# Kernel tuning notes

Measured on AMD Instinct MI355X. Metric: run time of the kernel, lower is better.

## Reference

```python
import jax, jax.numpy as jnp
import numpy as np

EPS = 1e-5

def _ln(x, g, b):
    m = jnp.mean(x, axis=-1, keepdims=True)
    v = jnp.mean(jnp.square(x - m), axis=-1, keepdims=True)
    return (x - m) * jax.lax.rsqrt(v + EPS) * g + b

def setup_inputs() -> dict:
    key = jax.random.key(0)
    ks = jax.random.split(key, 20)
    B, F = 262144, 768
    sizes = [F, 512, 256, 128, 1]  # LN(d_in) -> Linear(d_in, d_out) per block
    inp = {"input": jax.random.normal(ks[0], (B, F), dtype=jnp.float32)}
    for i in range(4):
        din, dout = sizes[i], sizes[i + 1]
        inp[f"g{i}"] = jnp.ones((din,), dtype=jnp.float32)
        inp[f"b{i}"] = jnp.zeros((din,), dtype=jnp.float32)
        bound = 1.0 / np.sqrt(din)
        inp[f"W{i}"] = jax.random.uniform(ks[1 + 2 * i], (dout, din), dtype=jnp.float32, minval=-bound, maxval=bound)
        inp[f"c{i}"] = jax.random.uniform(ks[2 + 2 * i], (dout,), dtype=jnp.float32, minval=-bound, maxval=bound)
    return inp

def reference(input, g0, b0, W0, c0, g1, b1, W1, c1, g2, b2, W2, c2, g3, b3, W3, c3):
    x = input
    params = [(g0, b0, W0, c0), (g1, b1, W1, c1), (g2, b2, W2, c2), (g3, b3, W3, c3)]
    for i, (g, b, W, c) in enumerate(params):
        x = _ln(x, g, b)
        x = x @ W.T + c
        if i != 3:
            x = jax.nn.elu(x)
    return jnp.squeeze(x, axis=-1)  # [B]
```

## Files before the change

### kernel.cpp

```cpp
#include <hip/hip_runtime.h>
#include <hip/hip_fp16.h>
#include <math.h>

typedef _Float16 half_t;
typedef half_t half4_t __attribute__((ext_vector_type(4)));
typedef half_t half8_t __attribute__((ext_vector_type(8)));
typedef float f32x4 __attribute__((ext_vector_type(4)));

#define LN_EPS 1e-5f

__global__ void pack_weights(const float* __restrict__ W0, const float* __restrict__ g0,
                             const float* __restrict__ W1, const float* __restrict__ g1,
                             const float* __restrict__ W2, const float* __restrict__ g2,
                             half_t* __restrict__ ws) {
    int sid = blockIdx.x * 256 + threadIdx.x;
    const float* W; const float* g; int K, T, off;
    if (sid < 49152)      { W = W0; g = g0; K = 768; T = 24; off = 0; }
    else if (sid < 65536) { W = W1; g = g1; K = 512; T = 16; off = 49152; sid -= 49152; }
    else if (sid < 69632) { W = W2; g = g2; K = 256; T = 8;  off = 65536; sid -= 65536; }
    else return;
    const int l   = sid & 63;
    const int t   = (sid >> 6) % T;
    const int cbg = (sid >> 6) / T;
    const int n   = (l & 15) + 16 * cbg;
    const int k0  = 32 * t + 8 * (l >> 4);
    const float* src = W + (size_t)n * K + k0;
    const float* gs  = g + k0;
    half8_t v;
    #pragma unroll
    for (int jq = 0; jq < 8; jq++) v[jq] = (half_t)(src[jq] * gs[jq]);
    *(half8_t*)(ws + (size_t)(off + sid) * 8) = v;
}

__global__ void fold_bias(const float* __restrict__ W0, const float* __restrict__ g0,
                          const float* __restrict__ b0, const float* __restrict__ c0,
                          const float* __restrict__ W1, const float* __restrict__ g1,
                          const float* __restrict__ b1, const float* __restrict__ c1,
                          const float* __restrict__ W2, const float* __restrict__ g2,
                          const float* __restrict__ b2, const float* __restrict__ c2,
                          const float* __restrict__ W3, const float* __restrict__ g3,
                          const float* __restrict__ b3, const float* __restrict__ c3,
                          float* __restrict__ f) {
    const int gw   = (blockIdx.x * 256 + threadIdx.x) >> 6;
    const int lane = threadIdx.x & 63;
    if (gw == 896) {
        float s = 0.f, cb_ = 0.f;
        for (int k = lane; k < 128; k += 64) {
            const float wg = W3[k] * g3[k];
            f[1792 + k] = wg;
            s += wg; cb_ += W3[k] * b3[k];
        }
        #pragma unroll
        for (int m = 1; m < 64; m <<= 1) { s += __shfl_xor(s, m); cb_ += __shfl_xor(cb_, m); }
        if (lane == 0) { f[1920] = s; f[1921] = cb_ + c3[0]; }
        return;
    }
    const float *W, *g, *b, *cc; int K, n; float *sf, *cf;
    if (gw < 512)      { W = W0; g = g0; b = b0; cc = c0; K = 768; n = gw;       sf = f;        cf = f + 512; }
    else if (gw < 768) { W = W1; g = g1; b = b1; cc = c1; K = 512; n = gw - 512; sf = f + 1024; cf = f + 1280; }
    else if (gw < 896) { W = W2; g = g2; b = b2; cc = c2; K = 256; n = gw - 768; sf = f + 1536; cf = f + 1664; }
    else return;
    const float* Wr = W + (size_t)n * K;
    float s = 0.f, cb_ = 0.f;
    for (int k = lane; k < K; k += 64) { const float wg = Wr[k] * g[k]; s += wg; cb_ += Wr[k] * b[k]; }
    #pragma unroll
    for (int m = 1; m < 64; m <<= 1) { s += __shfl_xor(s, m); cb_ += __shfl_xor(cb_, m); }
    if (lane == 0) { sf[n] = s; cf[n] = cb_ + cc[n]; }
}

__global__ __launch_bounds__(512, 4)
void fused_mlp(const float* __restrict__ x_in,
               const half_t* __restrict__ W0p, const half_t* __restrict__ W1p,
               const half_t* __restrict__ W2p, const float* __restrict__ f,
               float* __restrict__ out)
{
    __shared__ half_t frag[32768];
    __shared__ float psum[8][64], psq[8][64], pdot[8][64];
    __shared__ float row_m[64], row_rs[64];

    const int tid  = threadIdx.x;
    const int lane = tid & 63;
    const int wv   = tid >> 6;
    const int grp  = lane >> 4;
    const int cl   = lane & 15;
    const int row  = tid >> 3;
    const int jj   = tid & 7;
    const int rbw  = row >> 4;
    const long r0  = (long)blockIdx.x * 64;
    const float* xrow = x_in + (r0 + row) * 768;

    const float* s0f = f;        const float* c0f = f + 512;
    const float* s1f = f + 1024; const float* c1f = f + 1280;
    const float* s2f = f + 1536; const float* c2f = f + 1664;
    const float* w3f = f + 1792;

    float s = 0.f, ss = 0.f;
    f32x4 vb[4];

    auto stage_load = [&](int c) {
        const float* xp = xrow + 128 * c + 4 * jj;
        #pragma unroll
        for (int i = 0; i < 4; i++)
            vb[i] = __builtin_nontemporal_load((const f32x4*)(xp + 32 * i));
    };
    auto stage_write = [&](int c) {
        half_t* fb = frag + 8192 * (c & 1);
        const int hg = jj >> 1, jo = 4 * (jj & 1);
        #pragma unroll
        for (int i = 0; i < 4; i++) {
            const f32x4 v = vb[i];
            s  += v[0] + v[1] + v[2] + v[3];
            ss += v[0]*v[0] + v[1]*v[1] + v[2]*v[2] + v[3]*v[3];
            half4_t hv;
            hv[0] = (half_t)v[0]; hv[1] = (half_t)v[1];
            hv[2] = (half_t)v[2]; hv[3] = (half_t)v[3];
            *(half4_t*)(&fb[((i * 4 + rbw) * 64 + ((row & 15) + 16 * hg)) * 8 + jo]) = hv;
        }
    };

    f32x4 acc0[4][4];
    #pragma unroll
    for (int rb = 0; rb < 4; rb++)
        #pragma unroll
        for (int cb = 0; cb < 4; cb++) acc0[rb][cb] = 0.f;

    auto gemm0 = [&](int c) {
        const half_t* fb = frag + 8192 * (c & 1);
        const half_t* wp = W0p + (size_t)(4 * wv * 24 + 4 * c) * 512 + lane * 8;
        half8_t bA[4], bB[4];
        #pragma unroll
        for (int cb = 0; cb < 4; cb++) bA[cb] = *(const half8_t*)(wp + cb * 12288);
        #pragma unroll
        for (int tt = 0; tt < 4; tt++) {
            half8_t* cur = (tt & 1) ? bB : bA;
            half8_t* nxt = (tt & 1) ? bA : bB;
            if (tt < 3) {
                #pragma unroll
                for (int cb = 0; cb < 4; cb++)
                    nxt[cb] = *(const half8_t*)(wp + (tt + 1) * 512 + cb * 12288);
            }
            half8_t af[4];
            #pragma unroll
            for (int rb = 0; rb < 4; rb++)
                af[rb] = *(const half8_t*)(&fb[((tt * 4 + rb) * 64 + lane) * 8]);
            #pragma unroll
            for (int cb = 0; cb < 4; cb++)
                #pragma unroll
                for (int rb = 0; rb < 4; rb++)
                    acc0[rb][cb] = __builtin_amdgcn_mfma_f32_16x16x32_f16(af[rb], cur[cb], acc0[rb][cb], 0, 0, 0);
        }
    };

    stage_load(0); stage_write(0);
    __syncthreads();
    #pragma unroll 1
    for (int c = 0; c < 6; c++) {
        if (c < 5) stage_load(c + 1);
        gemm0(c);
        if (c < 5) stage_write(c + 1);
        if (c == 4) {
            s  += __shfl_xor(s, 1);  s  += __shfl_xor(s, 2);  s  += __shfl_xor(s, 4);
            ss += __shfl_xor(ss, 1); ss += __shfl_xor(ss, 2); ss += __shfl_xor(ss, 4);
            if (jj == 0) {
                const float mm = s * (1.f / 768.f);
                row_m[row]  = mm;
                row_rs[row] = 1.f / sqrtf(ss * (1.f / 768.f) - mm * mm + LN_EPS);
            }
        }
        __syncthreads();
    }

    {
        float sv[4], cv[4];
        #pragma unroll
        for (int cb = 0; cb < 4; cb++) {
            const int c = cl + 16 * (4 * wv + cb);
            sv[cb] = s0f[c]; cv[cb] = c0f[c];
        }
        #pragma unroll
        for (int rb = 0; rb < 4; rb++)
            #pragma unroll
            for (int v = 0; v < 4; v++) {
                const int r = 16 * rb + 4 * grp + v;
                const float rm = row_m[r], rr = row_rs[r];
                float a_ = 0.f, q_ = 0.f;
                #pragma unroll
                for (int cb = 0; cb < 4; cb++) {
                    float y = rr * (acc0[rb][cb][v] - rm * sv[cb]) + cv[cb];
                    y = y > 0.f ? y : (__expf(y) - 1.f);
                    acc0[rb][cb][v] = y;
                    a_ += y; q_ += y * y;
                }
                a_ += __shfl_xor(a_, 1); a_ += __shfl_xor(a_, 2); a_ += __shfl_xor(a_, 4); a_ += __shfl_xor(a_, 8);
                q_ += __shfl_xor(q_, 1); q_ += __shfl_xor(q_, 2); q_ += __shfl_xor(q_, 4); q_ += __shfl_xor(q_, 8);
                if (cl == 0) { psum[wv][r] = a_; psq[wv][r] = q_; }
            }
        #pragma unroll
        for (int cb = 0; cb < 4; cb++) {
            const int c = cl + 16 * (4 * wv + cb);
            const int t = c >> 5, j = c & 7, sc = 16 * ((c >> 3) & 3);
            #pragma unroll
            for (int rb = 0; rb < 4; rb++)
                #pragma unroll
                for (int v = 0; v < 4; v++)
                    frag[((t * 4 + rb) * 64 + (4 * grp + v + sc)) * 8 + j] = (half_t)acc0[rb][cb][v];
        }
    }
    __syncthreads();
    if (tid < 64) {
        float a_ = 0.f, q_ = 0.f;
        #pragma unroll
        for (int w = 0; w < 8; w++) { a_ += psum[w][tid]; q_ += psq[w][tid]; }
        const float mm = a_ * (1.f / 512.f);
        row_m[tid]  = mm;
        row_rs[tid] = 1.f / sqrtf(q_ * (1.f / 512.f) - mm * mm + LN_EPS);
    }
    __syncthreads();

    f32x4 acc1[4][2];
    #pragma unroll
    for (int rb = 0; rb < 4; rb++) { acc1[rb][0] = 0.f; acc1[rb][1] = 0.f; }
    {
        const half_t* wp = W1p + (size_t)(2 * wv * 16) * 512 + lane * 8;
        half8_t bA[2], bB[2];
        bA[0] = *(const half8_t*)(wp);
        bA[1] = *(const half8_t*)(wp + 8192);
        #pragma unroll
        for (int t = 0; t < 16; t++) {
            half8_t* cur = (t & 1) ? bB : bA;
            half8_t* nxt = (t & 1) ? bA : bB;
            if (t < 15) {
                nxt[0] = *(const half8_t*)(wp + (t + 1) * 512);
                nxt[1] = *(const half8_t*)(wp + (t + 1) * 512 + 8192);
            }
            half8_t af[4];
            #pragma unroll
            for (int rb = 0; rb < 4; rb++)
                af[rb] = *(const half8_t*)(&frag[((t * 4 + rb) * 64 + lane) * 8]);
            #pragma unroll
            for (int cb = 0; cb < 2; cb++)
                #pragma unroll
                for (int rb = 0; rb < 4; rb++)
                    acc1[rb][cb] = __builtin_amdgcn_mfma_f32_16x16x32_f16(af[rb], cur[cb], acc1[rb][cb], 0, 0, 0);
        }
    }

    {
        float sv[2], cv[2];
        #pragma unroll
        for (int cb = 0; cb < 2; cb++) {
            const int c = cl + 16 * (2 * wv + cb);
            sv[cb] = s1f[c]; cv[cb] = c1f[c];
        }
        #pragma unroll
        for (int rb = 0; rb < 4; rb++)
            #pragma unroll
            for (int v = 0; v < 4; v++) {
                const int r = 16 * rb + 4 * grp + v;
                const float rm = row_m[r], rr = row_rs[r];
                float a_ = 0.f, q_ = 0.f;
                #pragma unroll
                for (int cb = 0; cb < 2; cb++) {
                    float y = rr * (acc1[rb][cb][v] - rm * sv[cb]) + cv[cb];
                    y = y > 0.f ? y : (__expf(y) - 1.f);
                    acc1[rb][cb][v] = y;
                    a_ += y; q_ += y * y;
                }
                a_ += __shfl_xor(a_, 1); a_ += __shfl_xor(a_, 2); a_ += __shfl_xor(a_, 4); a_ += __shfl_xor(a_, 8);
                q_ += __shfl_xor(q_, 1); q_ += __shfl_xor(q_, 2); q_ += __shfl_xor(q_, 4); q_ += __shfl_xor(q_, 8);
                if (cl == 0) { psum[wv][r] = a_; psq[wv][r] = q_; }
            }
    }
    __syncthreads();
    #pragma unroll
    for (int cb = 0; cb < 2; cb++) {
        const int c = cl + 16 * (2 * wv + cb);
        const int t = c >> 5, j = c & 7, sc = 16 * ((c >> 3) & 3);
        #pragma unroll
        for (int rb = 0; rb < 4; rb++)
            #pragma unroll
            for (int v = 0; v < 4; v++)
                frag[((t * 4 + rb) * 64 + (4 * grp + v + sc)) * 8 + j] = (half_t)acc1[rb][cb][v];
    }
    if (tid < 64) {
        float a_ = 0.f, q_ = 0.f;
        #pragma unroll
        for (int w = 0; w < 8; w++) { a_ += psum[w][tid]; q_ += psq[w][tid]; }
        const float mm = a_ * (1.f / 256.f);
        row_m[tid]  = mm;
        row_rs[tid] = 1.f / sqrtf(q_ * (1.f / 256.f) - mm * mm + LN_EPS);
    }
    __syncthreads();

    f32x4 acc2[4];
    #pragma unroll
    for (int rb = 0; rb < 4; rb++) acc2[rb] = 0.f;
    {
        const half_t* wp = W2p + (size_t)(wv * 8) * 512 + lane * 8;
        half8_t bA = *(const half8_t*)(wp);
        #pragma unroll
        for (int t = 0; t < 8; t++) {
            const half8_t cur = bA;
            if (t < 7) bA = *(const half8_t*)(wp + (t + 1) * 512);
            half8_t af[4];
            #pragma unroll
            for (int rb = 0; rb < 4; rb++)
                af[rb] = *(const half8_t*)(&frag[((t * 4 + rb) * 64 + lane) * 8]);
            #pragma unroll
            for (int rb = 0; rb < 4; rb++)
                acc2[rb] = __builtin_amdgcn_mfma_f32_16x16x32_f16(af[rb], cur, acc2[rb], 0, 0, 0);
        }
    }

    {
        const int c2i = cl + 16 * wv;
        const float sv = s2f[c2i], cv = c2f[c2i], w3v = w3f[c2i];
        #pragma unroll
        for (int rb = 0; rb < 4; rb++)
            #pragma unroll
            for (int v = 0; v < 4; v++) {
                const int r = 16 * rb + 4 * grp + v;
                const float rm = row_m[r], rr = row_rs[r];
                float y = rr * (acc2[rb][v] - rm * sv) + cv;
                y = y > 0.f ? y : (__expf(y) - 1.f);
                float a_ = y, q_ = y * y, d_ = y * w3v;
                a_ += __shfl_xor(a_, 1); a_ += __shfl_xor(a_, 2); a_ += __shfl_xor(a_, 4); a_ += __shfl_xor(a_, 8);
                q_ += __shfl_xor(q_, 1); q_ += __shfl_xor(q_, 2); q_ += __shfl_xor(q_, 4); q_ += __shfl_xor(q_, 8);
                d_ += __shfl_xor(d_, 1); d_ += __shfl_xor(d_, 2); d_ += __shfl_xor(d_, 4); d_ += __shfl_xor(d_, 8);
                if (cl == 0) { psum[wv][r] = a_; psq[wv][r] = q_; pdot[wv][r] = d_; }
            }
    }
    __syncthreads();
    if (tid < 64) {
        float a_ = 0.f, q_ = 0.f, d_ = 0.f;
        #pragma unroll
        for (int w = 0; w < 8; w++) { a_ += psum[w][tid]; q_ += psq[w][tid]; d_ += pdot[w][tid]; }
        const float mm = a_ * (1.f / 128.f);
        const float rs = 1.f / sqrtf(q_ * (1.f / 128.f) - mm * mm + LN_EPS);
        out[r0 + tid] = rs * (d_ - mm * f[1920]) + f[1921];
    }
}

extern "C" void kernel_launch(void* const* d_in, const int* in_sizes, int n_in,
                              void* d_out, int out_size, void* d_ws, size_t ws_size,
                              hipStream_t stream) {
    const float* x  = (const float*)d_in[0];
    const float* g0 = (const float*)d_in[1];
    const float* b0 = (const float*)d_in[2];
    const float* W0 = (const float*)d_in[3];
    const float* c0 = (const float*)d_in[4];
    const float* g1 = (const float*)d_in[5];
    const float* b1 = (const float*)d_in[6];
    const float* W1 = (const float*)d_in[7];
    const float* c1 = (const float*)d_in[8];
    const float* g2 = (const float*)d_in[9];
    const float* b2 = (const float*)d_in[10];
    const float* W2 = (const float*)d_in[11];
    const float* c2 = (const float*)d_in[12];
    const float* g3 = (const float*)d_in[13];
    const float* b3 = (const float*)d_in[14];
    const float* W3 = (const float*)d_in[15];
    const float* c3 = (const float*)d_in[16];

    half_t* ws = (half_t*)d_ws;
    float*  f  = (float*)(ws + 557056);

    pack_weights<<<272, 256, 0, stream>>>(W0, g0, W1, g1, W2, g2, ws);
    fold_bias<<<225, 256, 0, stream>>>(W0, g0, b0, c0, W1, g1, b1, c1,
                                       W2, g2, b2, c2, W3, g3, b3, c3, f);

    const int nrows = in_sizes[0] / 768;
    fused_mlp<<<nrows / 64, 512, 0, stream>>>(
        x, ws, ws + 393216, ws + 524288, f, (float*)d_out);
}
```

Measured before the change: 577.7 us.

## Compute per-row LayerNorm stats from half-precision LDS fragments instead of shuffles

Per-row mean and variance for the next LayerNorm are now computed after activations are written to shared memory. Eight threads per row read the half-precision fragments and reduce with 3-step shuffles, replacing per-wave 4-step shuffle reductions plus cross-wave partial-sum arrays and a serial 64-thread combine. This removes a block barrier per layer and the single-wave tail reduction, but it adds LDS reads and uses fp16-rounded values for the statistics. The final layer stages outputs in a padded LDS tile and caches the last weight vector in shared memory.

```diff
diff --git a/kernel.cpp b/kernel.cpp
--- a/kernel.cpp
+++ b/kernel.cpp
@@ -75,8 +75,8 @@
                float* __restrict__ out)
 {
     __shared__ half_t frag[32768];
-    __shared__ float psum[8][64], psq[8][64], pdot[8][64];
     __shared__ float row_m[64], row_rs[64];
+    __shared__ float w3s[128];
 
     const int tid  = threadIdx.x;
     const int lane = tid & 63;
@@ -92,7 +92,8 @@
     const float* s0f = f;        const float* c0f = f + 512;
     const float* s1f = f + 1024; const float* c1f = f + 1280;
     const float* s2f = f + 1536; const float* c2f = f + 1664;
-    const float* w3f = f + 1792;
+
+    if (tid < 128) w3s[tid] = f[1792 + tid];
 
     float s = 0.f, ss = 0.f;
     f32x4 vb[4];
@@ -183,17 +184,11 @@
             for (int v = 0; v < 4; v++) {
                 const int r = 16 * rb + 4 * grp + v;
                 const float rm = row_m[r], rr = row_rs[r];
-                float a_ = 0.f, q_ = 0.f;
                 #pragma unroll
                 for (int cb = 0; cb < 4; cb++) {
                     float y = rr * (acc0[rb][cb][v] - rm * sv[cb]) + cv[cb];
-                    y = y > 0.f ? y : (__expf(y) - 1.f);
-                    acc0[rb][cb][v] = y;
-                    a_ += y; q_ += y * y;
+                    acc0[rb][cb][v] = y > 0.f ? y : (__expf(y) - 1.f);
                 }
-                a_ += __shfl_xor(a_, 1); a_ += __shfl_xor(a_, 2); a_ += __shfl_xor(a_, 4); a_ += __shfl_xor(a_, 8);
-                q_ += __shfl_xor(q_, 1); q_ += __shfl_xor(q_, 2); q_ += __shfl_xor(q_, 4); q_ += __shfl_xor(q_, 8);
-                if (cl == 0) { psum[wv][r] = a_; psq[wv][r] = q_; }
             }
         #pragma unroll
         for (int cb = 0; cb < 4; cb++) {
@@ -207,15 +202,26 @@
         }
     }
     __syncthreads();
-    if (tid < 64) {
-        float a_ = 0.f, q_ = 0.f;
-        #pragma unroll
-        for (int w = 0; w < 8; w++) { a_ += psum[w][tid]; q_ += psq[w][tid]; }
-        const float mm = a_ * (1.f / 512.f);
-        row_m[tid]  = mm;
-        row_rs[tid] = 1.f / sqrtf(q_ * (1.f / 512.f) - mm * mm + LN_EPS);
-    }
-    __syncthreads();
+
+    {
+        const int r15 = row & 15, rb = row >> 4;
+        float s_ = 0.f, q_ = 0.f;
+        #pragma unroll
+        for (int i = 0; i < 8; i++) {
+            const int ch = jj + 8 * i;
+            const int t = ch >> 2, cg = ch & 3;
+            const half8_t h = *(const half8_t*)(frag + (size_t)((t * 4 + rb) * 64 + r15 + 16 * cg) * 8);
+            #pragma unroll
+            for (int e = 0; e < 8; e++) { const float fv = (float)h[e]; s_ += fv; q_ += fv * fv; }
+        }
+        s_ += __shfl_xor(s_, 1); s_ += __shfl_xor(s_, 2); s_ += __shfl_xor(s_, 4);
+        q_ += __shfl_xor(q_, 1); q_ += __shfl_xor(q_, 2); q_ += __shfl_xor(q_, 4);
+        if (jj == 0) {
+            const float mm = s_ * (1.f / 512.f);
+            row_m[row]  = mm;
+            row_rs[row] = 1.f / sqrtf(q_ * (1.f / 512.f) - mm * mm + LN_EPS);
+        }
+    }
 
     f32x4 acc1[4][2];
     #pragma unroll
@@ -244,6 +250,7 @@
                     acc1[rb][cb] = __builtin_amdgcn_mfma_f32_16x16x32_f16(af[rb], cur[cb], acc1[rb][cb], 0, 0, 0);
         }
     }
+    __syncthreads();
 
     {
         float sv[2], cv[2];
@@ -258,39 +265,44 @@
             for (int v = 0; v < 4; v++) {
                 const int r = 16 * rb + 4 * grp + v;
                 const float rm = row_m[r], rr = row_rs[r];
-                float a_ = 0.f, q_ = 0.f;
                 #pragma unroll
                 for (int cb = 0; cb < 2; cb++) {
                     float y = rr * (acc1[rb][cb][v] - rm * sv[cb]) + cv[cb];
-                    y = y > 0.f ? y : (__expf(y) - 1.f);
-                    acc1[rb][cb][v] = y;
-                    a_ += y; q_ += y * y;
+                    acc1[rb][cb][v] = y > 0.f ? y : (__expf(y) - 1.f);
                 }
-                a_ += __shfl_xor(a_, 1); a_ += __shfl_xor(a_, 2); a_ += __shfl_xor(a_, 4); a_ += __shfl_xor(a_, 8);
-                q_ += __shfl_xor(q_, 1); q_ += __shfl_xor(q_, 2); q_ += __shfl_xor(q_, 4); q_ += __shfl_xor(q_, 8);
-                if (cl == 0) { psum[wv][r] = a_; psq[wv][r] = q_; }
-            }
-    }
-    __syncthreads();
-    #pragma unroll
-    for (int cb = 0; cb < 2; cb++) {
-        const int c = cl + 16 * (2 * wv + cb);
-        const int t = c >> 5, j = c & 7, sc = 16 * ((c >> 3) & 3);
-        #pragma unroll
-        for (int rb = 0; rb < 4; rb++)
-            #pragma unroll
-            for (int v = 0; v < 4; v++)
-                frag[((t * 4 + rb) * 64 + (4 * grp + v + sc)) * 8 + j] = (half_t)acc1[rb][cb][v];
-    }
-    if (tid < 64) {
-        float a_ = 0.f, q_ = 0.f;
-        #pragma unroll
-        for (int w = 0; w < 8; w++) { a_ += psum[w][tid]; q_ += psq[w][tid]; }
-        const float mm = a_ * (1.f / 256.f);
-        row_m[tid]  = mm;
-        row_rs[tid] = 1.f / sqrtf(q_ * (1.f / 256.f) - mm * mm + LN_EPS);
-    }
-    __syncthreads();
+            }
+        #pragma unroll
+        for (int cb = 0; cb < 2; cb++) {
+            const int c = cl + 16 * (2 * wv + cb);
+            const int t = c >> 5, j = c & 7, sc = 16 * ((c >> 3) & 3);
+            #pragma unroll
+            for (int rb = 0; rb < 4; rb++)
+                #pragma unroll
+                for (int v = 0; v < 4; v++)
+                    frag[((t * 4 + rb) * 64 + (4 * grp + v + sc)) * 8 + j] = (half_t)acc1[rb][cb][v];
+        }
+    }
+    __syncthreads();
+
+    {
+        const int r15 = row & 15, rb = row >> 4;
+        float s_ = 0.f, q_ = 0.f;
+        #pragma unroll
+        for (int i = 0; i < 4; i++) {
+            const int ch = jj + 8 * i;
+            const int t = ch >> 2, cg = ch & 3;
+            const half8_t h = *(const half8_t*)(frag + (size_t)((t * 4 + rb) * 64 + r15 + 16 * cg) * 8);
+            #pragma unroll
+            for (int e = 0; e < 8; e++) { const float fv = (float)h[e]; s_ += fv; q_ += fv * fv; }
+        }
+        s_ += __shfl_xor(s_, 1); s_ += __shfl_xor(s_, 2); s_ += __shfl_xor(s_, 4);
+        q_ += __shfl_xor(q_, 1); q_ += __shfl_xor(q_, 2); q_ += __shfl_xor(q_, 4);
+        if (jj == 0) {
+            const float mm = s_ * (1.f / 256.f);
+            row_m[row]  = mm;
+            row_rs[row] = 1.f / sqrtf(q_ * (1.f / 256.f) - mm * mm + LN_EPS);
+        }
+    }
 
     f32x4 acc2[4];
     #pragma unroll
@@ -311,10 +323,11 @@
                 acc2[rb] = __builtin_amdgcn_mfma_f32_16x16x32_f16(af[rb], cur, acc2[rb], 0, 0, 0);
         }
     }
+    __syncthreads();
 
     {
         const int c2i = cl + 16 * wv;
-        const float sv = s2f[c2i], cv = c2f[c2i], w3v = w3f[c2i];
+        const float sv = s2f[c2i], cv = c2f[c2i];
         #pragma unroll
         for (int rb = 0; rb < 4; rb++)
             #pragma unroll
@@ -323,21 +336,31 @@
                 const float rm = row_m[r], rr = row_rs[r];
                 float y = rr * (acc2[rb][v] - rm * sv) + cv;
                 y = y > 0.f ? y : (__expf(y) - 1.f);
-                float a_ = y, q_ = y * y, d_ = y * w3v;
-                a_ += __shfl_xor(a_, 1); a_ += __shfl_xor(a_, 2); a_ += __shfl_xor(a_, 4); a_ += __shfl_xor(a_, 8);
-                q_ += __shfl_xor(q_, 1); q_ += __shfl_xor(q_, 2); q_ += __shfl_xor(q_, 4); q_ += __shfl_xor(q_, 8);
-                d_ += __shfl_xor(d_, 1); d_ += __shfl_xor(d_, 2); d_ += __shfl_xor(d_, 4); d_ += __shfl_xor(d_, 8);
-                if (cl == 0) { psum[wv][r] = a_; psq[wv][r] = q_; pdot[wv][r] = d_; }
-            }
-    }
-    __syncthreads();
-    if (tid < 64) {
-        float a_ = 0.f, q_ = 0.f, d_ = 0.f;
-        #pragma unroll
-        for (int w = 0; w < 8; w++) { a_ += psum[w][tid]; q_ += psq[w][tid]; d_ += pdot[w][tid]; }
-        const float mm = a_ * (1.f / 128.f);
-        const float rs = 1.f / sqrtf(q_ * (1.f / 128.f) - mm * mm + LN_EPS);
-        out[r0 + tid] = rs * (d_ - mm * f[1920]) + f[1921];
+                frag[r * 136 + c2i] = (half_t)y;
+            }
+    }
+    __syncthreads();
+
+    {
+        float s_ = 0.f, q_ = 0.f, d_ = 0.f;
+        #pragma unroll
+        for (int u = 0; u < 2; u++) {
+            const int cb = jj * 16 + 8 * u;
+            const half8_t h = *(const half8_t*)(frag + row * 136 + cb);
+            #pragma unroll
+            for (int e = 0; e < 8; e++) {
+                const float fv = (float)h[e];
+                s_ += fv; q_ += fv * fv; d_ += fv * w3s[cb + e];
+            }
+        }
+        s_ += __shfl_xor(s_, 1); s_ += __shfl_xor(s_, 2); s_ += __shfl_xor(s_, 4);
+        q_ += __shfl_xor(q_, 1); q_ += __shfl_xor(q_, 2); q_ += __shfl_xor(q_, 4);
+        d_ += __shfl_xor(d_, 1); d_ += __shfl_xor(d_, 2); d_ += __shfl_xor(d_, 4);
+        if (jj == 0) {
+            const float mm = s_ * (1.f / 128.f);
+            const float rs = 1.f / sqrtf(q_ * (1.f / 128.f) - mm * mm + LN_EPS);
+            out[r0 + row] = rs * (d_ - mm * f[1920]) + f[1921];
+        }
     }
 }
 
```

Result: faster. 548.0 us (-5.1%).

## Process two row tiles per block, overlapping tile B loads with tile A tail layers

Applied to the files above, without the earlier changes.

Each block now handles 128 rows as two 64-row tiles. The layer-1/2/3 GEMMs and epilogues of tile A are interleaved with the streaming x loads and layer-0 GEMM chunks of tile B, so the memory-bound input stream overlaps the small tail layers. The LN0 statistics and the final LN3/dot are computed with fp16 fdot2 instead of fp32 FMAs, and the last layer's reduction now goes through shared memory rather than shuffles plus a cross-wave reduction. Occupancy hint drops to 2 blocks per CU and LDS grows, and fp16 statistics accumulation may reduce accuracy.

```diff
diff --git a/kernel.cpp b/kernel.cpp
--- a/kernel.cpp
+++ b/kernel.cpp
@@ -3,11 +3,13 @@
 #include <math.h>
 
 typedef _Float16 half_t;
+typedef half_t half2_t __attribute__((ext_vector_type(2)));
 typedef half_t half4_t __attribute__((ext_vector_type(4)));
 typedef half_t half8_t __attribute__((ext_vector_type(8)));
 typedef float f32x4 __attribute__((ext_vector_type(4)));
 
 #define LN_EPS 1e-5f
+#define FDOT2(a, b, c) __builtin_amdgcn_fdot2((a), (b), (c), false)
 
 __global__ void pack_weights(const float* __restrict__ W0, const float* __restrict__ g0,
                              const float* __restrict__ W1, const float* __restrict__ g1,
@@ -68,15 +70,17 @@
     if (lane == 0) { sf[n] = s; cf[n] = cb_ + cc[n]; }
 }
 
-__global__ __launch_bounds__(512, 4)
+__global__ __launch_bounds__(512, 2)
 void fused_mlp(const float* __restrict__ x_in,
                const half_t* __restrict__ W0p, const half_t* __restrict__ W1p,
                const half_t* __restrict__ W2p, const float* __restrict__ f,
                float* __restrict__ out)
 {
-    __shared__ half_t frag[32768];
-    __shared__ float psum[8][64], psq[8][64], pdot[8][64];
-    __shared__ float row_m[64], row_rs[64];
+    __shared__ half_t xreg[32768];
+    __shared__ half_t stg2[16384];
+    __shared__ float rmA[64], rsA[64], rmB[64], rsB[64];
+    __shared__ float ps[8][64], pq[8][64];
+    __shared__ half2_t w3h[64];
 
     const int tid  = threadIdx.x;
     const int lane = tid & 63;
@@ -86,46 +90,64 @@
     const int row  = tid >> 3;
     const int jj   = tid & 7;
     const int rbw  = row >> 4;
-    const long r0  = (long)blockIdx.x * 64;
-    const float* xrow = x_in + (r0 + row) * 768;
+    const long r0  = (long)blockIdx.x * 128;
+    const float* xrA = x_in + (r0 + row) * 768;
+    const float* xrB = xrA + 64 * 768;
 
     const float* s0f = f;        const float* c0f = f + 512;
     const float* s1f = f + 1024; const float* c1f = f + 1280;
     const float* s2f = f + 1536; const float* c2f = f + 1664;
-    const float* w3f = f + 1792;
-
-    float s = 0.f, ss = 0.f;
+    const half2_t one2 = {(half_t)1.f, (half_t)1.f};
+
+    if (tid < 64) {
+        half2_t w; w[0] = (half_t)f[1792 + 2 * tid]; w[1] = (half_t)f[1793 + 2 * tid];
+        w3h[tid] = w;
+    }
+
+    float sA = 0.f, ssA = 0.f, sB = 0.f, ssB = 0.f;
     f32x4 vb[4];
-
-    auto stage_load = [&](int c) {
-        const float* xp = xrow + 128 * c + 4 * jj;
+    f32x4 acc0[4][4];
+    f32x4 acc1[4][2];
+    f32x4 acc2[4];
+
+    auto zacc0 = [&]() {
+        #pragma unroll
+        for (int rb = 0; rb < 4; rb++)
+            #pragma unroll
+            for (int cb = 0; cb < 4; cb++) acc0[rb][cb] = 0.f;
+    };
+
+    auto stage_load = [&](const float* xr, int c) {
+        const float* xp = xr + 128 * c + 4 * jj;
         #pragma unroll
         for (int i = 0; i < 4; i++)
             vb[i] = __builtin_nontemporal_load((const f32x4*)(xp + 32 * i));
     };
-    auto stage_write = [&](int c) {
-        half_t* fb = frag + 8192 * (c & 1);
+    auto stage_write = [&](int c, float& s_, float& ss_) {
+        half_t* fb = stg2 + 8192 * (c & 1);
         const int hg = jj >> 1, jo = 4 * (jj & 1);
         #pragma unroll
         for (int i = 0; i < 4; i++) {
             const f32x4 v = vb[i];
-            s  += v[0] + v[1] + v[2] + v[3];
-            ss += v[0]*v[0] + v[1]*v[1] + v[2]*v[2] + v[3]*v[3];
-            half4_t hv;
-            hv[0] = (half_t)v[0]; hv[1] = (half_t)v[1];
-            hv[2] = (half_t)v[2]; hv[3] = (half_t)v[3];
+            half2_t h01; h01[0] = (half_t)v[0]; h01[1] = (half_t)v[1];
+            half2_t h23; h23[0] = (half_t)v[2]; h23[1] = (half_t)v[3];
+            s_  = FDOT2(h01, one2, s_);  s_  = FDOT2(h23, one2, s_);
+            ss_ = FDOT2(h01, h01, ss_);  ss_ = FDOT2(h23, h23, ss_);
+            half4_t hv; hv[0] = h01[0]; hv[1] = h01[1]; hv[2] = h23[0]; hv[3] = h23[1];
             *(half4_t*)(&fb[((i * 4 + rbw) * 64 + ((row & 15) + 16 * hg)) * 8 + jo]) = hv;
         }
     };
-
-    f32x4 acc0[4][4];
-    #pragma unroll
-    for (int rb = 0; rb < 4; rb++)
-        #pragma unroll
-        for (int cb = 0; cb < 4; cb++) acc0[rb][cb] = 0.f;
-
-    auto gemm0 = [&](int c) {
-        const half_t* fb = frag + 8192 * (c & 1);
+    auto ln0_fin = [&](float& s_, float& ss_, float* rm, float* rs) {
+        s_  += __shfl_xor(s_, 1);  s_  += __shfl_xor(s_, 2);  s_  += __shfl_xor(s_, 4);
+        ss_ += __shfl_xor(ss_, 1); ss_ += __shfl_xor(ss_, 2); ss_ += __shfl_xor(ss_, 4);
+        if (jj == 0) {
+            const float mm = s_ * (1.f / 768.f);
+            rm[row] = mm;
+            rs[row] = 1.f / sqrtf(ss_ * (1.f / 768.f) - mm * mm + LN_EPS);
+        }
+    };
+    auto gemm0c = [&](int c) {
+        const half_t* fb = stg2 + 8192 * (c & 1);
         const half_t* wp = W0p + (size_t)(4 * wv * 24 + 4 * c) * 512 + lane * 8;
         half8_t bA[4], bB[4];
         #pragma unroll
@@ -150,27 +172,7 @@
                     acc0[rb][cb] = __builtin_amdgcn_mfma_f32_16x16x32_f16(af[rb], cur[cb], acc0[rb][cb], 0, 0, 0);
         }
     };
-
-    stage_load(0); stage_write(0);
-    __syncthreads();
-    #pragma unroll 1
-    for (int c = 0; c < 6; c++) {
-        if (c < 5) stage_load(c + 1);
-        gemm0(c);
-        if (c < 5) stage_write(c + 1);
-        if (c == 4) {
-            s  += __shfl_xor(s, 1);  s  += __shfl_xor(s, 2);  s  += __shfl_xor(s, 4);
-            ss += __shfl_xor(ss, 1); ss += __shfl_xor(ss, 2); ss += __shfl_xor(ss, 4);
-            if (jj == 0) {
-                const float mm = s * (1.f / 768.f);
-                row_m[row]  = mm;
-                row_rs[row] = 1.f / sqrtf(ss * (1.f / 768.f) - mm * mm + LN_EPS);
-            }
-        }
-        __syncthreads();
-    }
-
-    {
+    auto ep0 = [&](const float* rm0, const float* rs0) {
         float sv[4], cv[4];
         #pragma unroll
         for (int cb = 0; cb < 4; cb++) {
@@ -182,7 +184,7 @@
             #pragma unroll
             for (int v = 0; v < 4; v++) {
                 const int r = 16 * rb + 4 * grp + v;
-                const float rm = row_m[r], rr = row_rs[r];
+                const float rm = rm0[r], rr = rs0[r];
                 float a_ = 0.f, q_ = 0.f;
                 #pragma unroll
                 for (int cb = 0; cb < 4; cb++) {
@@ -193,7 +195,7 @@
                 }
                 a_ += __shfl_xor(a_, 1); a_ += __shfl_xor(a_, 2); a_ += __shfl_xor(a_, 4); a_ += __shfl_xor(a_, 8);
                 q_ += __shfl_xor(q_, 1); q_ += __shfl_xor(q_, 2); q_ += __shfl_xor(q_, 4); q_ += __shfl_xor(q_, 8);
-                if (cl == 0) { psum[wv][r] = a_; psq[wv][r] = q_; }
+                if (cl == 0) { ps[wv][r] = a_; pq[wv][r] = q_; }
             }
         #pragma unroll
         for (int cb = 0; cb < 4; cb++) {
@@ -203,24 +205,22 @@
             for (int rb = 0; rb < 4; rb++)
                 #pragma unroll
                 for (int v = 0; v < 4; v++)
-                    frag[((t * 4 + rb) * 64 + (4 * grp + v + sc)) * 8 + j] = (half_t)acc0[rb][cb][v];
-        }
-    }
-    __syncthreads();
-    if (tid < 64) {
-        float a_ = 0.f, q_ = 0.f;
-        #pragma unroll
-        for (int w = 0; w < 8; w++) { a_ += psum[w][tid]; q_ += psq[w][tid]; }
-        const float mm = a_ * (1.f / 512.f);
-        row_m[tid]  = mm;
-        row_rs[tid] = 1.f / sqrtf(q_ * (1.f / 512.f) - mm * mm + LN_EPS);
-    }
-    __syncthreads();
-
-    f32x4 acc1[4][2];
-    #pragma unroll
-    for (int rb = 0; rb < 4; rb++) { acc1[rb][0] = 0.f; acc1[rb][1] = 0.f; }
-    {
+                    xreg[((t * 4 + rb) * 64 + (4 * grp + v + sc)) * 8 + j] = (half_t)acc0[rb][cb][v];
+        }
+    };
+    auto combine = [&](float* rm, float* rs, float inv) {
+        if (tid < 64) {
+            float a_ = 0.f, q_ = 0.f;
+            #pragma unroll
+            for (int w = 0; w < 8; w++) { a_ += ps[w][tid]; q_ += pq[w][tid]; }
+            const float mm = a_ * inv;
+            rm[tid] = mm;
+            rs[tid] = 1.f / sqrtf(q_ * inv - mm * mm + LN_EPS);
+        }
+    };
+    auto gemm1 = [&]() {
+        #pragma unroll
+        for (int rb = 0; rb < 4; rb++) { acc1[rb][0] = 0.f; acc1[rb][1] = 0.f; }
         const half_t* wp = W1p + (size_t)(2 * wv * 16) * 512 + lane * 8;
         half8_t bA[2], bB[2];
         bA[0] = *(const half8_t*)(wp);
@@ -236,16 +236,15 @@
             half8_t af[4];
             #pragma unroll
             for (int rb = 0; rb < 4; rb++)
-                af[rb] = *(const half8_t*)(&frag[((t * 4 + rb) * 64 + lane) * 8]);
+                af[rb] = *(const half8_t*)(&xreg[((t * 4 + rb) * 64 + lane) * 8]);
             #pragma unroll
             for (int cb = 0; cb < 2; cb++)
                 #pragma unroll
                 for (int rb = 0; rb < 4; rb++)
                     acc1[rb][cb] = __builtin_amdgcn_mfma_f32_16x16x32_f16(af[rb], cur[cb], acc1[rb][cb], 0, 0, 0);
         }
-    }
-
-    {
+    };
+    auto ep1 = [&](const float* rm1, const float* rs1) {
         float sv[2], cv[2];
         #pragma unroll
         for (int cb = 0; cb < 2; cb++) {
@@ -257,7 +256,7 @@
             #pragma unroll
             for (int v = 0; v < 4; v++) {
                 const int r = 16 * rb + 4 * grp + v;
-                const float rm = row_m[r], rr = row_rs[r];
+                const float rm = rm1[r], rr = rs1[r];
                 float a_ = 0.f, q_ = 0.f;
                 #pragma unroll
                 for (int cb = 0; cb < 2; cb++) {
@@ -268,34 +267,22 @@
                 }
                 a_ += __shfl_xor(a_, 1); a_ += __shfl_xor(a_, 2); a_ += __shfl_xor(a_, 4); a_ += __shfl_xor(a_, 8);
                 q_ += __shfl_xor(q_, 1); q_ += __shfl_xor(q_, 2); q_ += __shfl_xor(q_, 4); q_ += __shfl_xor(q_, 8);
-                if (cl == 0) { psum[wv][r] = a_; psq[wv][r] = q_; }
+                if (cl == 0) { ps[wv][r] = a_; pq[wv][r] = q_; }
             }
-    }
-    __syncthreads();
-    #pragma unroll
-    for (int cb = 0; cb < 2; cb++) {
-        const int c = cl + 16 * (2 * wv + cb);
-        const int t = c >> 5, j = c & 7, sc = 16 * ((c >> 3) & 3);
-        #pragma unroll
-        for (int rb = 0; rb < 4; rb++)
-            #pragma unroll
-            for (int v = 0; v < 4; v++)
-                frag[((t * 4 + rb) * 64 + (4 * grp + v + sc)) * 8 + j] = (half_t)acc1[rb][cb][v];
-    }
-    if (tid < 64) {
-        float a_ = 0.f, q_ = 0.f;
-        #pragma unroll
-        for (int w = 0; w < 8; w++) { a_ += psum[w][tid]; q_ += psq[w][tid]; }
-        const float mm = a_ * (1.f / 256.f);
-        row_m[tid]  = mm;
-        row_rs[tid] = 1.f / sqrtf(q_ * (1.f / 256.f) - mm * mm + LN_EPS);
-    }
-    __syncthreads();
-
-    f32x4 acc2[4];
-    #pragma unroll
-    for (int rb = 0; rb < 4; rb++) acc2[rb] = 0.f;
-    {
+        #pragma unroll
+        for (int cb = 0; cb < 2; cb++) {
+            const int c = cl + 16 * (2 * wv + cb);
+            const int t = c >> 5, j = c & 7, sc = 16 * ((c >> 3) & 3);
+            #pragma unroll
+            for (int rb = 0; rb < 4; rb++)
+                #pragma unroll
+                for (int v = 0; v < 4; v++)
+                    xreg[((t * 4 + rb) * 64 + (4 * grp + v + sc)) * 8 + j] = (half_t)acc1[rb][cb][v];
+        }
+    };
+    auto gemm2 = [&]() {
+        #pragma unroll
+        for (int rb = 0; rb < 4; rb++) acc2[rb] = 0.f;
         const half_t* wp = W2p + (size_t)(wv * 8) * 512 + lane * 8;
         half8_t bA = *(const half8_t*)(wp);
         #pragma unroll
@@ -305,40 +292,112 @@
             half8_t af[4];
             #pragma unroll
             for (int rb = 0; rb < 4; rb++)
-                af[rb] = *(const half8_t*)(&frag[((t * 4 + rb) * 64 + lane) * 8]);
+                af[rb] = *(const half8_t*)(&xreg[((t * 4 + rb) * 64 + lane) * 8]);
             #pragma unroll
             for (int rb = 0; rb < 4; rb++)
                 acc2[rb] = __builtin_amdgcn_mfma_f32_16x16x32_f16(af[rb], cur, acc2[rb], 0, 0, 0);
         }
-    }
-
-    {
+    };
+    auto ep2 = [&](const float* rm2, const float* rs2) {
         const int c2i = cl + 16 * wv;
-        const float sv = s2f[c2i], cv = c2f[c2i], w3v = w3f[c2i];
+        const float sv = s2f[c2i], cv = c2f[c2i];
         #pragma unroll
         for (int rb = 0; rb < 4; rb++)
             #pragma unroll
             for (int v = 0; v < 4; v++) {
                 const int r = 16 * rb + 4 * grp + v;
-                const float rm = row_m[r], rr = row_rs[r];
+                const float rm = rm2[r], rr = rs2[r];
                 float y = rr * (acc2[rb][v] - rm * sv) + cv;
                 y = y > 0.f ? y : (__expf(y) - 1.f);
-                float a_ = y, q_ = y * y, d_ = y * w3v;
-                a_ += __shfl_xor(a_, 1); a_ += __shfl_xor(a_, 2); a_ += __shfl_xor(a_, 4); a_ += __shfl_xor(a_, 8);
-                q_ += __shfl_xor(q_, 1); q_ += __shfl_xor(q_, 2); q_ += __shfl_xor(q_, 4); q_ += __shfl_xor(q_, 8);
-                d_ += __shfl_xor(d_, 1); d_ += __shfl_xor(d_, 2); d_ += __shfl_xor(d_, 4); d_ += __shfl_xor(d_, 8);
-                if (cl == 0) { psum[wv][r] = a_; psq[wv][r] = q_; pdot[wv][r] = d_; }
+                xreg[r * 136 + c2i] = (half_t)y;
             }
+    };
+    auto lastout = [&](long rbase) {
+        float s_ = 0.f, q_ = 0.f, d_ = 0.f;
+        #pragma unroll
+        for (int u = 0; u < 2; u++) {
+            const int cb = jj * 16 + 8 * u;
+            const int wi = cb >> 1;
+            const half8_t h = *(const half8_t*)(xreg + row * 136 + cb);
+            half2_t p0 = {h[0], h[1]}, p1 = {h[2], h[3]}, p2 = {h[4], h[5]}, p3 = {h[6], h[7]};
+            s_ = FDOT2(p0, one2, s_); s_ = FDOT2(p1, one2, s_);
+            s_ = FDOT2(p2, one2, s_); s_ = FDOT2(p3, one2, s_);
+            q_ = FDOT2(p0, p0, q_);   q_ = FDOT2(p1, p1, q_);
+            q_ = FDOT2(p2, p2, q_);   q_ = FDOT2(p3, p3, q_);
+            d_ = FDOT2(p0, w3h[wi], d_);     d_ = FDOT2(p1, w3h[wi + 1], d_);
+            d_ = FDOT2(p2, w3h[wi + 2], d_); d_ = FDOT2(p3, w3h[wi + 3], d_);
+        }
+        s_ += __shfl_xor(s_, 1); s_ += __shfl_xor(s_, 2); s_ += __shfl_xor(s_, 4);
+        q_ += __shfl_xor(q_, 1); q_ += __shfl_xor(q_, 2); q_ += __shfl_xor(q_, 4);
+        d_ += __shfl_xor(d_, 1); d_ += __shfl_xor(d_, 2); d_ += __shfl_xor(d_, 4);
+        if (jj == 0) {
+            const float mm = s_ * (1.f / 128.f);
+            const float rs = 1.f / sqrtf(q_ * (1.f / 128.f) - mm * mm + LN_EPS);
+            out[rbase + row] = rs * (d_ - mm * f[1920]) + f[1921];
+        }
+    };
+
+    zacc0();
+    stage_load(xrA, 0); stage_write(0, sA, ssA);
+    __syncthreads();
+    #pragma unroll 1
+    for (int c = 0; c < 6; c++) {
+        if (c < 5) stage_load(xrA, c + 1);
+        gemm0c(c);
+        if (c < 5) stage_write(c + 1, sA, ssA);
+        if (c == 4) ln0_fin(sA, ssA, rmA, rsA);
+        __syncthreads();
     }
-    __syncthreads();
-    if (tid < 64) {
-        float a_ = 0.f, q_ = 0.f, d_ = 0.f;
-        #pragma unroll
-        for (int w = 0; w < 8; w++) { a_ += psum[w][tid]; q_ += psq[w][tid]; d_ += pdot[w][tid]; }
-        const float mm = a_ * (1.f / 128.f);
-        const float rs = 1.f / sqrtf(q_ * (1.f / 128.f) - mm * mm + LN_EPS);
-        out[r0 + tid] = rs * (d_ - mm * f[1920]) + f[1921];
-    }
+
+    stage_load(xrB, 0);
+    ep0(rmA, rsA);
+    stage_write(0, sB, ssB);
+    __syncthreads();
+    stage_load(xrB, 1);
+    combine(rmA, rsA, 1.f / 512.f);
+    zacc0();
+    gemm1();
+    gemm0c(0);
+    stage_write(1, sB, ssB);
+    __syncthreads();
+    stage_load(xrB, 2);
+    ep1(rmA, rsA);
+    gemm0c(1);
+    stage_write(2, sB, ssB);
+    __syncthreads();
+    stage_load(xrB, 3);
+    combine(rmA, rsA, 1.f / 256.f);
+    gemm2();
+    gemm0c(2);
+    stage_write(3, sB, ssB);
+    __syncthreads();
+    stage_load(xrB, 4);
+    ep2(rmA, rsA);
+    gemm0c(3);
+    stage_write(4, sB, ssB);
+    __syncthreads();
+    stage_load(xrB, 5);
+    lastout(r0);
+    gemm0c(4);
+    stage_write(5, sB, ssB);
+    ln0_fin(sB, ssB, rmB, rsB);
+    __syncthreads();
+    gemm0c(5);
+    __syncthreads();
+
+    ep0(rmB, rsB);
+    __syncthreads();
+    combine(rmB, rsB, 1.f / 512.f);
+    gemm1();
+    __syncthreads();
+    ep1(rmB, rsB);
+    __syncthreads();
+    combine(rmB, rsB, 1.f / 256.f);
+    gemm2();
+    __syncthreads();
+    ep2(rmB, rsB);
+    __syncthreads();
+    lastout(r0 + 64);
 }
 
 extern "C" void kernel_launch(void* const* d_in, const int* in_sizes, int n_in,
@@ -370,6 +429,6 @@
                                        W2, g2, b2, c2, W3, g3, b3, c3, f);
 
     const int nrows = in_sizes[0] / 768;
-    fused_mlp<<<nrows / 64, 512, 0, stream>>>(
+    fused_mlp<<<nrows / 128, 512, 0, stream>>>(
         x, ws, ws + 393216, ws + 524288, f, (float*)d_out);
 }
```

Result: faster. 482.4 us, median of 2 (-16.5%).
